# Kernel optimization log

Hardware: AMD Instinct MI355X
Metric: run time of the kernel (lower is better)

## Reference

```python
import jax, jax.numpy as jnp
import numpy as np

V, L, H, D, S, B = 32000, 6, 16, 1024, 512, 4
DK = D // H
DF = 4 * D
EPS = 1e-5


def setup_inputs() -> dict:
    key = jax.random.key(0)
    ks = jax.random.split(key, 24)
    std = 0.02
    def w(k, shape):
        return jax.random.normal(k, shape, dtype=jnp.float32) * std
    inp = {
        'x': jax.random.randint(ks[0], (B, S), 0, V),
        'tok_emb': w(ks[1], (V, D)),
        # per-layer params stacked on leading L axis; Linear stored as [in,out]
        'wq': w(ks[2], (L, D, D)), 'bq': jnp.zeros((L, D)),
        'wk': w(ks[3], (L, D, D)), 'bk': jnp.zeros((L, D)),
        'wv': w(ks[4], (L, D, D)), 'bv': jnp.zeros((L, D)),
        'wo': w(ks[5], (L, D, D)), 'bo': jnp.zeros((L, D)),
        'ln1_g': jnp.ones((L, D)), 'ln1_b': jnp.zeros((L, D)),
        'w1': w(ks[6], (L, D, DF)), 'b1': jnp.zeros((L, DF)),
        'w2': w(ks[7], (L, DF, D)), 'b2': jnp.zeros((L, D)),
        'ln2_g': jnp.ones((L, D)), 'ln2_b': jnp.zeros((L, D)),
        'lnf_g': jnp.ones((D,)), 'lnf_b': jnp.zeros((D,)),
        'lm_w': w(ks[8], (D, V)),
    }
    return inp


def _layernorm(x, g, b):
    mu = jnp.mean(x, axis=-1, keepdims=True)
    var = jnp.mean(jnp.square(x - mu), axis=-1, keepdims=True)
    return (x - mu) * jax.lax.rsqrt(var + EPS) * g + b


def _sinusoidal_pe(seq_len, d_model):
    pos = jnp.arange(seq_len, dtype=jnp.float32)[:, None]
    div = jnp.exp(jnp.arange(0, d_model, 2, dtype=jnp.float32) * (-np.log(10000.0) / d_model))
    pe = jnp.zeros((seq_len, d_model), dtype=jnp.float32)
    pe = pe.at[:, 0::2].set(jnp.sin(pos * div))
    pe = pe.at[:, 1::2].set(jnp.cos(pos * div))
    return pe  # [S, D]


def _gpt_forward(x, tok_emb, wq, bq, wk, bk, wv, bv, wo, bo,
                 ln1_g, ln1_b, w1, b1, w2, b2, ln2_g, ln2_b,
                 lnf_g, lnf_b, lm_w):
    b, s = x.shape
    h = tok_emb[x] + _sinusoidal_pe(s, D)  # [B,S,D]
    causal = jnp.tril(jnp.ones((s, s), dtype=bool))  # True = keep
    scale = 1.0 / np.sqrt(DK)

    def block(h, p):
        (wq, bq, wk, bk, wv, bv, wo, bo,
         ln1_g, ln1_b, w1, b1, w2, b2, ln2_g, ln2_b) = p
        hn = _layernorm(h, ln1_g, ln1_b)
        q = (hn @ wq + bq).reshape(b, s, H, DK)
        k = (hn @ wk + bk).reshape(b, s, H, DK)
        v = (hn @ wv + bv).reshape(b, s, H, DK)
        scores = jnp.einsum('bqhd,bkhd->bhqk', q, k) * scale
        scores = jnp.where(causal, scores, -1e9)
        attn = jax.nn.softmax(scores, axis=-1)
        ctx = jnp.einsum('bhqk,bkhd->bqhd', attn, v).reshape(b, s, D)
        h = h + (ctx @ wo + bo)
        hn2 = _layernorm(h, ln2_g, ln2_b)
        ff = jax.nn.gelu(hn2 @ w1 + b1, approximate=False) @ w2 + b2
        return h + ff, None

    params = (wq, bq, wk, bk, wv, bv, wo, bo,
              ln1_g, ln1_b, w1, b1, w2, b2, ln2_g, ln2_b)
    h, _ = jax.lax.scan(block, h, params)
    h = _layernorm(h, lnf_g, lnf_b)
    return h @ lm_w  # [B,S,V] logits


def reference(x, tok_emb, wq, bq, wk, bk, wv, bv, wo, bo,
              ln1_g, ln1_b, w1, b1, w2, b2, ln2_g, ln2_b,
              lnf_g, lnf_b, lm_w):
    return _gpt_forward(x, tok_emb, wq, bq, wk, bk, wv, bv, wo, bo,
                        ln1_g, ln1_b, w1, b1, w2, b2, ln2_g, ln2_b,
                        lnf_g, lnf_b, lm_w)
```

## Files before the change

### kernel.cpp

```cpp
#include <hip/hip_runtime.h>
#include <hip/hip_bf16.h>
#include <math.h>

#define V_SIZE 32000
#define L_NUM 6
#define H_NUM 16
#define D_MODEL 1024
#define S_LEN 512
#define B_SZ 4
#define DF_DIM 4096
#define ROWS (B_SZ * S_LEN)
#define QKV_N (3 * D_MODEL)
#define KVBLK 64
#define NJOB 12

typedef unsigned short u16;
typedef __attribute__((ext_vector_type(8))) short short8v;
typedef __attribute__((ext_vector_type(4))) float f32x4;

__device__ __forceinline__ float b2f(u16 b) {
  union { float f; unsigned u; } c; c.u = ((unsigned)b) << 16; return c.f;
}
__device__ __forceinline__ u16 f2b(float f) {
  __hip_bfloat16 h = __float2bfloat16(f);
  union { __hip_bfloat16 h; u16 u; } c; c.h = h; return c.u;
}
__device__ __forceinline__ void g2l16(const void* g, void* l) {
  __builtin_amdgcn_global_load_lds(
      (const __attribute__((address_space(1))) void*)g,
      (__attribute__((address_space(3))) void*)l, 16, 0, 0);
}

__global__ __launch_bounds__(256) void embed_kernel(
    const int* __restrict__ x, const float* __restrict__ tok_emb,
    float* __restrict__ h) {
  int row = blockIdx.x;
  int s = row % S_LEN;
  int tok = x[row];
  const float* te = tok_emb + (size_t)tok * D_MODEL;
  float* hr = h + (size_t)row * D_MODEL;
  float pos = (float)s;
  const float c = 9.210340371976184f / (float)D_MODEL;
#pragma unroll
  for (int i = 0; i < D_MODEL / 256; ++i) {
    int d = threadIdx.x + i * 256;
    float freq = expf(-(float)(d & ~1) * c);
    float ang = pos * freq;
    float pe = (d & 1) ? cosf(ang) : sinf(ang);
    hr[d] = te[d] + pe;
  }
}

__global__ __launch_bounds__(256) void layernorm_kernel(
    const float* __restrict__ in, const float* __restrict__ g,
    const float* __restrict__ b, u16* __restrict__ out) {
  const int row = blockIdx.x * 4 + (threadIdx.x >> 6);
  const int lane = threadIdx.x & 63;
  const float4* xr = (const float4*)(in + (size_t)row * D_MODEL);
  float4 v[4];
  float s1 = 0.f, s2 = 0.f;
#pragma unroll
  for (int i = 0; i < 4; ++i) {
    float4 t = xr[lane + i * 64];
    v[i] = t;
    s1 += t.x + t.y + t.z + t.w;
    s2 += t.x * t.x + t.y * t.y + t.z * t.z + t.w * t.w;
  }
#pragma unroll
  for (int off = 32; off; off >>= 1) {
    s1 += __shfl_xor(s1, off, 64);
    s2 += __shfl_xor(s2, off, 64);
  }
  const float mu = s1 * (1.0f / D_MODEL);
  const float var = s2 * (1.0f / D_MODEL) - mu * mu;
  const float rstd = rsqrtf(var + 1e-5f);
  u16* orow = out + (size_t)row * D_MODEL;
#pragma unroll
  for (int i = 0; i < 4; ++i) {
    const int d = (lane + i * 64) * 4;
    const float4 gv = *(const float4*)&g[d];
    const float4 bv = *(const float4*)&b[d];
    u16 o0 = f2b((v[i].x - mu) * rstd * gv.x + bv.x);
    u16 o1 = f2b((v[i].y - mu) * rstd * gv.y + bv.y);
    u16 o2 = f2b((v[i].z - mu) * rstd * gv.z + bv.z);
    u16 o3 = f2b((v[i].w - mu) * rstd * gv.w + bv.w);
    uint2 pk;
    pk.x = (unsigned)o0 | ((unsigned)o1 << 16);
    pk.y = (unsigned)o2 | ((unsigned)o3 << 16);
    *(uint2*)&orow[d] = pk;
  }
}

__global__ __launch_bounds__(256) void transpose_all(
    const float* __restrict__ wq, const float* __restrict__ wk,
    const float* __restrict__ wv, const float* __restrict__ wo,
    const float* __restrict__ w1, const float* __restrict__ w2,
    const float* __restrict__ lm_w,
    u16* __restrict__ wqkvT, u16* __restrict__ woT,
    u16* __restrict__ w1T, u16* __restrict__ w2T, u16* __restrict__ lmT) {
  const size_t DD = (size_t)D_MODEL * D_MODEL;
  const size_t DDF = (size_t)D_MODEL * DF_DIM;
  const long QS = (long)QKV_N * D_MODEL;
  int gid = blockIdx.x;
  const float* src;
  u16* dst;
  int K, N, kt, nt;
  if (gid < 12288) {
    const int l = gid / 2048, rjob = gid % 2048;
    const int which = rjob / 512, t = rjob % 512;
    kt = t % 16; nt = t / 16;
    K = D_MODEL; N = D_MODEL;
    src = (which == 0 ? wq : which == 1 ? wk : which == 2 ? wv : wo) + l * DD;
    dst = (which < 3) ? (wqkvT + l * QS + which * DD) : (woT + l * DD);
  } else if (gid < 24576) {
    const int idx = gid - 12288;
    const int l = idx / 2048, t = idx % 2048;
    kt = t % 16; nt = t / 16;
    K = D_MODEL; N = DF_DIM;
    src = w1 + l * DDF; dst = w1T + l * DDF;
  } else if (gid < 36864) {
    const int idx = gid - 24576;
    const int l = idx / 2048, t = idx % 2048;
    kt = t % 64; nt = t / 64;
    K = DF_DIM; N = D_MODEL;
    src = w2 + l * DDF; dst = w2T + l * DDF;
  } else {
    const int idx = gid - 36864;
    kt = idx % 16; nt = idx / 16;
    K = D_MODEL; N = V_SIZE;
    src = lm_w; dst = lmT;
  }
  __shared__ float t[64][33];
  const int n0 = nt * 32, k0 = kt * 64;
  const int tx = threadIdx.x & 31, ty = threadIdx.x >> 5;
#pragma unroll
  for (int i = 0; i < 64; i += 8)
    t[ty + i][tx] = src[(size_t)(k0 + ty + i) * N + n0 + tx];
  __syncthreads();
#pragma unroll
  for (int j = 0; j < 32; j += 8) {
    const int n = ty + j;
    u16 lo = f2b(t[2 * tx][n]);
    u16 hi = f2b(t[2 * tx + 1][n]);
    *(unsigned*)&dst[(size_t)(n0 + n) * K + k0 + 2 * tx] =
        (unsigned)lo | ((unsigned)hi << 16);
  }
}

__global__ __launch_bounds__(256) void pack_qkv_bias(
    const float* __restrict__ bq, const float* __restrict__ bk,
    const float* __restrict__ bv, float* __restrict__ out) {
  int i = blockIdx.x * 256 + threadIdx.x;
  int l = i / QKV_N, j = i % QKV_N;
  float v = (j < D_MODEL) ? bq[l * D_MODEL + j]
          : (j < 2 * D_MODEL) ? bk[l * D_MODEL + j - D_MODEL]
          : bv[l * D_MODEL + j - 2 * D_MODEL];
  out[i] = v;
}

template <int TM, int OUT_MODE, bool GELU_ACT, int SPLITK>
__global__ __launch_bounds__(256) void gemm_bf16(
    const u16* __restrict__ A, const u16* __restrict__ Bt,
    const float* __restrict__ bias, float* __restrict__ Cf,
    u16* __restrict__ Cb, int M, int N, int K) {
  constexpr int MF = TM / 32;
  constexpr int AINSTS = TM / 32;
  __shared__ __align__(16) u16 As[2][TM * 64];
  __shared__ __align__(16) u16 Bs[2][128 * 64];
  const int tid = threadIdx.x;
  const int wid = tid >> 6;
  const int lane = tid & 63;
  const int wr = wid >> 1, wc = wid & 1;
  const int nwg = gridDim.x;
  const int id = blockIdx.x;
  const int q = nwg >> 3, r = nwg & 7;
  const int xcd = id & 7, i0 = id >> 3;
  const int swz = (xcd < r ? xcd * (q + 1) : r * (q + 1) + (xcd - r) * q) + i0;
  const int kh = (SPLITK > 1) ? (swz & (SPLITK - 1)) : 0;
  const int rest = (SPLITK > 1) ? (swz >> 1) : swz;
  const int gm = M / TM;
  const int bm = rest % gm, bn = rest / gm;
  const int Ksub = K / SPLITK;
  const int rowi = lane >> 3;
  const int gsw = ((lane & 7) ^ rowi) * 8;
  const u16* Ag = A + (size_t)(bm * TM + wid * (TM / 4) + rowi) * K + kh * Ksub + gsw;
  const u16* Bg = Bt + (size_t)(bn * 128 + wid * 32 + rowi) * K + kh * Ksub + gsw;
  auto stage = [&](int buf, int k0) {
#pragma unroll
    for (int i = 0; i < AINSTS; ++i)
      g2l16(Ag + k0 + (size_t)(8 * i) * K, As[buf] + wid * (TM / 4) * 64 + i * 512);
#pragma unroll
    for (int i = 0; i < 4; ++i)
      g2l16(Bg + k0 + (size_t)(8 * i) * K, Bs[buf] + wid * 2048 + i * 512);
  };
  f32x4 acc[MF][4] = {};
  const int fr = lane & 15;
  const int hi = lane >> 4;
  stage(0, 0);
  __syncthreads();
  for (int k0 = 0; k0 < Ksub; k0 += 64) {
    const int cur = (k0 >> 6) & 1;
    if (k0 + 64 < Ksub) stage(cur ^ 1, k0 + 64);
    short8v a[MF][2], b[4][2];
#pragma unroll
    for (int m = 0; m < MF; ++m)
#pragma unroll
      for (int kk = 0; kk < 2; ++kk) {
        const int g = (kk * 4 + hi) ^ (fr & 7);
        a[m][kk] = *(const short8v*)&As[cur][(wr * (TM / 2) + m * 16 + fr) * 64 + g * 8];
      }
#pragma unroll
    for (int n = 0; n < 4; ++n)
#pragma unroll
      for (int kk = 0; kk < 2; ++kk) {
        const int g = (kk * 4 + hi) ^ (fr & 7);
        b[n][kk] = *(const short8v*)&Bs[cur][(wc * 64 + n * 16 + fr) * 64 + g * 8];
      }
    __builtin_amdgcn_s_setprio(1);
#pragma unroll
    for (int kk = 0; kk < 2; ++kk)
#pragma unroll
      for (int m = 0; m < MF; ++m)
#pragma unroll
        for (int n = 0; n < 4; ++n)
          acc[m][n] = __builtin_amdgcn_mfma_f32_16x16x32_bf16(a[m][kk], b[n][kk], acc[m][n], 0, 0, 0);
    __builtin_amdgcn_s_setprio(0);
    __syncthreads();
  }
  const int row0 = bm * TM + wr * (TM / 2) + hi * 4;
  const int col0 = bn * 128 + wc * 64 + fr;
#pragma unroll
  for (int m = 0; m < MF; ++m) {
#pragma unroll
    for (int n = 0; n < 4; ++n) {
      const int col = col0 + n * 16;
      float bv = (OUT_MODE == 2) ? 0.f : bias[col];
      if (SPLITK > 1 && kh != 0) bv = 0.f;
#pragma unroll
      for (int r2 = 0; r2 < 4; ++r2) {
        const int row = row0 + m * 16 + r2;
        float v = acc[m][n][r2] + bv;
        if (GELU_ACT) v = 0.5f * v * (1.0f + erff(v * 0.70710678118f));
        size_t idx = (size_t)row * N + col;
        if (OUT_MODE == 0) Cb[idx] = f2b(v);
        else if (OUT_MODE == 1) {
          if (SPLITK > 1) atomicAdd(&Cf[idx], v);
          else Cf[idx] += v;
        } else Cf[idx] = v;
      }
    }
  }
}

#define LDA_H(H)                                                            \
  _Pragma("unroll") for (int m = 0; m < 4; ++m)                             \
  _Pragma("unroll") for (int ks = 0; ks < 2; ++ks) {                        \
    const int row_ = wm * 128 + (H)*64 + m * 16 + fr;                       \
    const int g_ = (ks * 4 + hi) ^ (fr & 7);                                \
    a[m][ks] = *(const short8v*)&smem[cur * 16384 + row_ * 64 + g_ * 8];    \
  }
#define LDB_H(H)                                                            \
  _Pragma("unroll") for (int n = 0; n < 2; ++n)                             \
  _Pragma("unroll") for (int ks = 0; ks < 2; ++ks) {                        \
    const int row_ = wn * 64 + (H)*32 + n * 16 + fr;                        \
    const int g_ = (ks * 4 + hi) ^ (fr & 7);                                \
    b[n][ks] = *(const short8v*)&smem[32768 + cur * 16384 + row_ * 64 + g_ * 8]; \
  }
#define MFMA_CLUSTER(QA, QB)                                                \
  __builtin_amdgcn_s_barrier();                                             \
  asm volatile("s_waitcnt lgkmcnt(0)" ::: "memory");                        \
  __builtin_amdgcn_sched_barrier(0);                                        \
  __builtin_amdgcn_s_setprio(1);                                            \
  _Pragma("unroll") for (int ks = 0; ks < 2; ++ks)                          \
  _Pragma("unroll") for (int m = 0; m < 4; ++m)                             \
  _Pragma("unroll") for (int n = 0; n < 2; ++n)                             \
    acc[(QA)*4 + m][(QB)*2 + n] = __builtin_amdgcn_mfma_f32_16x16x32_bf16(  \
        a[m][ks], b[n][ks], acc[(QA)*4 + m][(QB)*2 + n], 0, 0, 0);          \
  __builtin_amdgcn_s_setprio(0);

__global__ __launch_bounds__(512, 2) void gemm256_lm(
    const u16* __restrict__ A, const u16* __restrict__ Bt,
    float* __restrict__ C, int M, int N, int K) {
  extern __shared__ __align__(16) u16 smem[];
  const int tid = threadIdx.x, wid = tid >> 6, lane = tid & 63;
  const int wm = wid >> 2, wn = wid & 3;
  const int fr = lane & 15, hi = lane >> 4;
  const int T = K / 64;
  const int nwg = gridDim.x, id = blockIdx.x;
  const int q = nwg >> 3, r = nwg & 7;
  const int xcd = id & 7, i0 = id >> 3;
  const int swz = (xcd < r ? xcd * (q + 1) : r * (q + 1) + (xcd - r) * q) + i0;
  const int gm = M / 256;
  const int bm = swz % gm, bn = swz / gm;
  const int rowA0 = bm * 256, rowB0 = bn * 256;
  const int rowoff = wid * 8 + (lane >> 3);
  const int gsw = ((lane & 7) ^ (lane >> 3)) * 8;
  auto stA = [&](int qq, int tt, int bb) {
    g2l16(A + (size_t)(rowA0 + qq * 64 + rowoff) * K + tt * 64 + gsw,
          smem + bb * 16384 + qq * 4096 + wid * 512);
  };
  auto stB = [&](int qq, int tt, int bb) {
    g2l16(Bt + (size_t)(rowB0 + qq * 64 + rowoff) * K + tt * 64 + gsw,
          smem + 32768 + bb * 16384 + qq * 4096 + wid * 512);
  };
  f32x4 acc[8][4] = {};
  stA(0, 0, 0); stA(2, 0, 0);
  stB(0, 0, 0); stB(1, 0, 0); stB(2, 0, 0); stB(3, 0, 0);
  stA(1, 0, 0); stA(3, 0, 0);
  if (T > 1) {
    stA(0, 1, 1); stA(2, 1, 1);
    asm volatile("s_waitcnt vmcnt(2)" ::: "memory");
  } else {
    asm volatile("s_waitcnt vmcnt(0)" ::: "memory");
  }
  __builtin_amdgcn_s_barrier();
  for (int t = 0; t < T; ++t) {
    const int cur = t & 1, nxt = cur ^ 1;
    short8v a[4][2], b[2][2];
    LDA_H(0); LDB_H(0);
    if (t + 1 < T) { stB(0, t + 1, nxt); stB(1, t + 1, nxt); }
    MFMA_CLUSTER(0, 0);
    __builtin_amdgcn_s_barrier();
    LDB_H(1);
    if (t + 1 < T) { stB(2, t + 1, nxt); stB(3, t + 1, nxt); }
    MFMA_CLUSTER(0, 1);
    __builtin_amdgcn_s_barrier();
    LDA_H(1);
    if (t + 1 < T) { stA(1, t + 1, nxt); stA(3, t + 1, nxt); }
    MFMA_CLUSTER(1, 1);
    __builtin_amdgcn_s_barrier();
    LDB_H(0);
    if (t + 2 < T) { stA(0, t + 2, cur); stA(2, t + 2, cur); }
    MFMA_CLUSTER(1, 0);
    if (t + 1 < T) {
      if (t + 2 < T) asm volatile("s_waitcnt vmcnt(2)" ::: "memory");
      else           asm volatile("s_waitcnt vmcnt(0)" ::: "memory");
      __builtin_amdgcn_s_barrier();
    }
  }
  float* lf = (float*)smem;
#pragma unroll
  for (int c = 0; c < 2; ++c) {
    __syncthreads();
    if (wm == c) {
#pragma unroll
      for (int m = 0; m < 8; ++m)
#pragma unroll
        for (int n = 0; n < 4; ++n)
#pragma unroll
          for (int rr = 0; rr < 4; ++rr)
            lf[(m * 16 + hi * 4 + rr) * 256 + wn * 64 + n * 16 + fr] =
                acc[m][n][rr];
    }
    __syncthreads();
#pragma unroll
    for (int i = 0; i < 16; ++i) {
      const int f = i * 2048 + tid * 4;
      const int rw = f >> 8, cl = f & 255;
      f32x4 v = *(const f32x4*)&lf[f];
      *(f32x4*)&C[(size_t)(rowA0 + c * 128 + rw) * N + rowB0 + cl] = v;
    }
  }
}

__global__ __launch_bounds__(256) void attn_part(
    const u16* __restrict__ qkv, float* __restrict__ Op,
    float* __restrict__ Ml, u16* __restrict__ ctx) {
  __shared__ __align__(16) u16 smem[3 * 64 * 72];
  u16 (*Qs)[72] = (u16(*)[72])smem;
  u16 (*Ks)[72] = (u16(*)[72])(smem + 4608);
  u16 (*Vs)[72] = (u16(*)[72])(smem + 9216);
  const int job = blockIdx.x, bh = blockIdx.y;
  constexpr int qt_of[NJOB] = {0, 1, 2, 3, 4, 4, 5, 5, 6, 6, 7, 7};
  constexpr int ch_of[NJOB] = {0, 0, 0, 0, 0, 1, 0, 1, 0, 1, 0, 1};
  const int qt = qt_of[job], ch = ch_of[job];
  const int b = bh >> 4, h = bh & 15;
  const int tid = threadIdx.x, wid = tid >> 6, lane = tid & 63;
  const int fr = lane & 15, ko = (lane >> 4) * 8;
  u16 (*Ps)[72] = (u16(*)[72])(smem + wid * 1152);
  const size_t rb = (size_t)b * S_LEN;
  const int q0 = qt * 64;
  const int hq = h * 64;
  const int t_lo = ch * 4;
  const int t_hi = (qt + 1 < t_lo + 4) ? qt + 1 : t_lo + 4;
#pragma unroll
  for (int i = 0; i < 2; ++i) {
    int e = tid + i * 256, r = e >> 3, c = (e & 7) * 8;
    *(short8v*)&Qs[r][c] = *(const short8v*)&qkv[(rb + q0 + r) * QKV_N + hq + c];
  }
  __syncthreads();
  short8v qf[2];
#pragma unroll
  for (int ks = 0; ks < 2; ++ks)
    qf[ks] = *(const short8v*)&Qs[wid * 16 + fr][ks * 32 + ko];
  f32x4 acc_o[4] = {};
  float mrow[4], lrow[4];
#pragma unroll
  for (int r = 0; r < 4; ++r) { mrow[r] = -1e30f; lrow[r] = 0.f; }
  short8v kreg[2], vreg[2];
  auto loadregs = [&](int t) {
    const int k0 = t * KVBLK;
#pragma unroll
    for (int i = 0; i < 2; ++i) {
      const int e = tid + i * 256, rr = e >> 3, cc = (e & 7) * 8;
      kreg[i] = *(const short8v*)&qkv[(rb + k0 + rr) * QKV_N + D_MODEL + hq + cc];
      vreg[i] = *(const short8v*)&qkv[(rb + k0 + rr) * QKV_N + 2 * D_MODEL + hq + cc];
    }
  };
  loadregs(t_lo);
  for (int t = t_lo; t < t_hi; ++t) {
    __syncthreads();
#pragma unroll
    for (int i = 0; i < 2; ++i) {
      const int e = tid + i * 256, rr = e >> 3, cc = (e & 7) * 8;
      *(short8v*)&Ks[rr][cc] = kreg[i];
#pragma unroll
      for (int j = 0; j < 8; ++j) Vs[cc + j][rr] = (u16)vreg[i][j];
    }
    __syncthreads();
    if (t + 1 < t_hi) loadregs(t + 1);
    const int k0 = t * KVBLK;
    f32x4 s[4] = {};
    __builtin_amdgcn_s_setprio(1);
#pragma unroll
    for (int n = 0; n < 4; ++n)
#pragma unroll
      for (int ks = 0; ks < 2; ++ks) {
        short8v kf = *(const short8v*)&Ks[n * 16 + fr][ks * 32 + ko];
        s[n] = __builtin_amdgcn_mfma_f32_16x16x32_bf16(qf[ks], kf, s[n], 0, 0, 0);
      }
    __builtin_amdgcn_s_setprio(0);
    const int rbase = q0 + wid * 16 + (lane >> 4) * 4;
#pragma unroll
    for (int r = 0; r < 4; ++r) {
      const int row_g = rbase + r;
      float vmax = -1e30f;
#pragma unroll
      for (int n = 0; n < 4; ++n) {
        float v = s[n][r] * 0.125f;
        if (k0 + n * 16 + fr > row_g) v = -1e30f;
        s[n][r] = v;
        vmax = fmaxf(vmax, v);
      }
#pragma unroll
      for (int off = 1; off < 16; off <<= 1) vmax = fmaxf(vmax, __shfl_xor(vmax, off, 64));
      const float mnew = fmaxf(mrow[r], vmax);
      const float sc = __expf(mrow[r] - mnew);
      mrow[r] = mnew;
      float ssum = 0.f;
#pragma unroll
      for (int n = 0; n < 4; ++n) {
        float p = __expf(s[n][r] - mnew);
        s[n][r] = p;
        ssum += p;
      }
#pragma unroll
      for (int off = 1; off < 16; off <<= 1) ssum += __shfl_xor(ssum, off, 64);
      lrow[r] = lrow[r] * sc + ssum;
#pragma unroll
      for (int n = 0; n < 4; ++n) {
        acc_o[n][r] *= sc;
        Ps[(lane >> 4) * 4 + r][n * 16 + fr] = f2b(s[n][r]);
      }
    }
    __builtin_amdgcn_s_setprio(1);
#pragma unroll
    for (int ks = 0; ks < 2; ++ks) {
      short8v pf = *(const short8v*)&Ps[fr][ks * 32 + ko];
#pragma unroll
      for (int n = 0; n < 4; ++n) {
        short8v vf = *(const short8v*)&Vs[n * 16 + fr][ks * 32 + ko];
        acc_o[n] = __builtin_amdgcn_mfma_f32_16x16x32_bf16(pf, vf, acc_o[n], 0, 0, 0);
      }
    }
    __builtin_amdgcn_s_setprio(0);
  }
  if (qt < 4) {
#pragma unroll
    for (int r = 0; r < 4; ++r) {
      const int row_l = wid * 16 + (lane >> 4) * 4 + r;
      const float inv = 1.0f / lrow[r];
#pragma unroll
      for (int n = 0; n < 4; ++n)
        ctx[(rb + q0 + row_l) * D_MODEL + hq + n * 16 + fr] = f2b(acc_o[n][r] * inv);
    }
  } else {
    const size_t jb = (size_t)(bh * NJOB + job);
#pragma unroll
    for (int r = 0; r < 4; ++r) {
      const int row_l = wid * 16 + (lane >> 4) * 4 + r;
      const size_t base = (jb * 64 + row_l) * 64;
#pragma unroll
      for (int n = 0; n < 4; ++n) Op[base + n * 16 + fr] = acc_o[n][r];
      if (fr == 0) {
        Ml[jb * 128 + row_l * 2] = mrow[r];
        Ml[jb * 128 + row_l * 2 + 1] = lrow[r];
      }
    }
  }
}

__global__ __launch_bounds__(256) void attn_combine(
    const float* __restrict__ Op, const float* __restrict__ Ml,
    u16* __restrict__ ctx) {
  const int qt = blockIdx.x + 4, bh = blockIdx.y;
  const int b = bh >> 4, h = bh & 15;
  const int j0 = 4 + blockIdx.x * 2;
  const size_t rb = (size_t)b * S_LEN;
  const int q0 = qt * 64, hq = h * 64;
  const size_t jb1 = (size_t)(bh * NJOB + j0);
  const size_t jb2 = jb1 + 1;
#pragma unroll
  for (int i = 0; i < 4; ++i) {
    const int idx4 = threadIdx.x + i * 256;
    const int row = idx4 >> 4, c4 = (idx4 & 15) * 4;
    f32x4 o1 = *(const f32x4*)&Op[(jb1 * 64 + row) * 64 + c4];
    const float m1 = Ml[jb1 * 128 + row * 2], l1 = Ml[jb1 * 128 + row * 2 + 1];
    f32x4 o2 = *(const f32x4*)&Op[(jb2 * 64 + row) * 64 + c4];
    const float m2 = Ml[jb2 * 128 + row * 2], l2 = Ml[jb2 * 128 + row * 2 + 1];
    const float m = fmaxf(m1, m2);
    const float e1 = __expf(m1 - m), e2 = __expf(m2 - m);
    const float inv = 1.0f / (l1 * e1 + l2 * e2);
    float o[4];
#pragma unroll
    for (int j = 0; j < 4; ++j) o[j] = o1[j] * e1 + o2[j] * e2;
    uint2 pk;
    pk.x = (unsigned)f2b(o[0] * inv) | ((unsigned)f2b(o[1] * inv) << 16);
    pk.y = (unsigned)f2b(o[2] * inv) | ((unsigned)f2b(o[3] * inv) << 16);
    *(uint2*)&ctx[(rb + q0 + row) * D_MODEL + hq + c4] = pk;
  }
}

extern "C" void kernel_launch(void* const* d_in, const int* in_sizes, int n_in,
                              void* d_out, int out_size, void* d_ws, size_t ws_size,
                              hipStream_t stream) {
  const int* x = (const int*)d_in[0];
  const float* tok_emb = (const float*)d_in[1];
  const float* wq = (const float*)d_in[2];
  const float* bq = (const float*)d_in[3];
  const float* wk = (const float*)d_in[4];
  const float* bk = (const float*)d_in[5];
  const float* wv = (const float*)d_in[6];
  const float* bv = (const float*)d_in[7];
  const float* wo = (const float*)d_in[8];
  const float* bo = (const float*)d_in[9];
  const float* ln1_g = (const float*)d_in[10];
  const float* ln1_b = (const float*)d_in[11];
  const float* w1 = (const float*)d_in[12];
  const float* b1 = (const float*)d_in[13];
  const float* w2 = (const float*)d_in[14];
  const float* b2 = (const float*)d_in[15];
  const float* ln2_g = (const float*)d_in[16];
  const float* ln2_b = (const float*)d_in[17];
  const float* lnf_g = (const float*)d_in[18];
  const float* lnf_b = (const float*)d_in[19];
  const float* lm_w = (const float*)d_in[20];

  char* w = (char*)d_ws;
  float* h    = (float*)(w);
  u16*  hn    = (u16*)(w + (8ll << 20));
  u16*  qkvb  = (u16*)(w + (12ll << 20));
  u16*  cbuf  = (u16*)(w + (24ll << 20));
  u16*  ff    = qkvb;
  u16*  wqkvT = (u16*)(w + (28ll << 20));
  u16*  woT   = (u16*)(w + (64ll << 20));
  u16*  w1T   = (u16*)(w + (76ll << 20));
  u16*  w2T   = (u16*)(w + (124ll << 20));
  u16*  lmT   = (u16*)(w + (172ll << 20));
  float* bqkv = (float*)(w + (235ll << 20));
  float* Op   = (float*)(w + (236ll << 20));
  float* Ml   = (float*)(w + (249ll << 20));

  transpose_all<<<52864, 256, 0, stream>>>(
      wq, wk, wv, wo, w1, w2, lm_w, wqkvT, woT, w1T, w2T, lmT);
  pack_qkv_bias<<<L_NUM * QKV_N / 256, 256, 0, stream>>>(bq, bk, bv, bqkv);

  embed_kernel<<<ROWS, 256, 0, stream>>>(x, tok_emb, h);

  const size_t DD = (size_t)D_MODEL * D_MODEL;
  const size_t DDF = (size_t)D_MODEL * DF_DIM;
  const long QS = (long)QKV_N * D_MODEL;
  const int nQKV = (ROWS / 64) * (QKV_N / 128);
  const int nPRJ = 2 * (ROWS / 64) * (D_MODEL / 128);
  const int nFF1 = (ROWS / 64) * (DF_DIM / 128);
  const int nFF2 = 2 * (ROWS / 64) * (D_MODEL / 128);
  for (int l = 0; l < L_NUM; ++l) {
    layernorm_kernel<<<ROWS / 4, 256, 0, stream>>>(h, ln1_g + l * D_MODEL, ln1_b + l * D_MODEL, hn);
    gemm_bf16<64, 0, false, 1><<<nQKV, 256, 0, stream>>>(
        hn, wqkvT + (size_t)l * QS, bqkv + l * QKV_N, nullptr, qkvb,
        ROWS, QKV_N, D_MODEL);
    attn_part<<<dim3(NJOB, B_SZ * H_NUM), 256, 0, stream>>>(qkvb, Op, Ml, cbuf);
    attn_combine<<<dim3(4, B_SZ * H_NUM), 256, 0, stream>>>(Op, Ml, cbuf);
    gemm_bf16<64, 1, false, 2><<<nPRJ, 256, 0, stream>>>(
        cbuf, woT + l * DD, bo + l * D_MODEL, h, nullptr, ROWS, D_MODEL, D_MODEL);
    layernorm_kernel<<<ROWS / 4, 256, 0, stream>>>(h, ln2_g + l * D_MODEL, ln2_b + l * D_MODEL, hn);
    gemm_bf16<64, 0, true, 1><<<nFF1, 256, 0, stream>>>(
        hn, w1T + l * DDF, b1 + l * DF_DIM, nullptr, ff, ROWS, DF_DIM, D_MODEL);
    gemm_bf16<64, 1, false, 2><<<nFF2, 256, 0, stream>>>(
        ff, w2T + l * DDF, b2 + l * D_MODEL, h, nullptr, ROWS, D_MODEL, DF_DIM);
  }
  layernorm_kernel<<<ROWS / 4, 256, 0, stream>>>(h, lnf_g, lnf_b, hn);

  hipFuncSetAttribute((const void*)gemm256_lm,
                      hipFuncAttributeMaxDynamicSharedMemorySize, 131072);
  const int nLM = (ROWS / 256) * (V_SIZE / 256);
  gemm256_lm<<<nLM, 512, 131072, stream>>>(
      hn, lmT, (float*)d_out, ROWS, V_SIZE, D_MODEL);
}
```

Measured before the change: 1.350 ms.

## Shrink LM-head GEMM tile to 128x256 with K=32 steps and higher occupancy

Replaces the 256x256 LM-head GEMM, which used 128KB of dynamic LDS and a K=64 pipelined schedule, with a 128x256 tile using K=32 steps and 48KB of static LDS. Launch bounds now allow 4 blocks per CU instead of 2, and the grid doubles. The goal is more resident waves and better latency hiding on the large vocab projection. In exchange, each block reuses less of its loaded data, a simpler double buffer waits on vmcnt(0) every iteration, and the fp32 output goes through LDS in four 32-row chunks.

```diff
diff --git a/kernel.cpp b/kernel.cpp
--- a/kernel.cpp
+++ b/kernel.cpp
@@ -252,113 +252,95 @@
   }
 }
 
-#define LDA_H(H)                                                            \
-  _Pragma("unroll") for (int m = 0; m < 4; ++m)                             \
-  _Pragma("unroll") for (int ks = 0; ks < 2; ++ks) {                        \
-    const int row_ = wm * 128 + (H)*64 + m * 16 + fr;                       \
-    const int g_ = (ks * 4 + hi) ^ (fr & 7);                                \
-    a[m][ks] = *(const short8v*)&smem[cur * 16384 + row_ * 64 + g_ * 8];    \
-  }
-#define LDB_H(H)                                                            \
-  _Pragma("unroll") for (int n = 0; n < 2; ++n)                             \
-  _Pragma("unroll") for (int ks = 0; ks < 2; ++ks) {                        \
-    const int row_ = wn * 64 + (H)*32 + n * 16 + fr;                        \
-    const int g_ = (ks * 4 + hi) ^ (fr & 7);                                \
-    b[n][ks] = *(const short8v*)&smem[32768 + cur * 16384 + row_ * 64 + g_ * 8]; \
-  }
-#define MFMA_CLUSTER(QA, QB)                                                \
-  __builtin_amdgcn_s_barrier();                                             \
-  asm volatile("s_waitcnt lgkmcnt(0)" ::: "memory");                        \
-  __builtin_amdgcn_sched_barrier(0);                                        \
-  __builtin_amdgcn_s_setprio(1);                                            \
-  _Pragma("unroll") for (int ks = 0; ks < 2; ++ks)                          \
-  _Pragma("unroll") for (int m = 0; m < 4; ++m)                             \
-  _Pragma("unroll") for (int n = 0; n < 2; ++n)                             \
-    acc[(QA)*4 + m][(QB)*2 + n] = __builtin_amdgcn_mfma_f32_16x16x32_bf16(  \
-        a[m][ks], b[n][ks], acc[(QA)*4 + m][(QB)*2 + n], 0, 0, 0);          \
-  __builtin_amdgcn_s_setprio(0);
-
-__global__ __launch_bounds__(512, 2) void gemm256_lm(
+__global__ __launch_bounds__(512, 4) void gemm_lm(
     const u16* __restrict__ A, const u16* __restrict__ Bt,
     float* __restrict__ C, int M, int N, int K) {
-  extern __shared__ __align__(16) u16 smem[];
+  __shared__ __align__(16) u16 smem[24576];
   const int tid = threadIdx.x, wid = tid >> 6, lane = tid & 63;
   const int wm = wid >> 2, wn = wid & 3;
   const int fr = lane & 15, hi = lane >> 4;
-  const int T = K / 64;
+  const int T = K / 32;
   const int nwg = gridDim.x, id = blockIdx.x;
   const int q = nwg >> 3, r = nwg & 7;
   const int xcd = id & 7, i0 = id >> 3;
   const int swz = (xcd < r ? xcd * (q + 1) : r * (q + 1) + (xcd - r) * q) + i0;
-  const int gm = M / 256;
+  const int gm = M / 128;
   const int bm = swz % gm, bn = swz / gm;
-  const int rowA0 = bm * 256, rowB0 = bn * 256;
-  const int rowoff = wid * 8 + (lane >> 3);
-  const int gsw = ((lane & 7) ^ (lane >> 3)) * 8;
-  auto stA = [&](int qq, int tt, int bb) {
-    g2l16(A + (size_t)(rowA0 + qq * 64 + rowoff) * K + tt * 64 + gsw,
-          smem + bb * 16384 + qq * 4096 + wid * 512);
+  const int rowA0 = bm * 128, rowB0 = bn * 256;
+  const int gsw = ((lane & 3) ^ ((lane >> 2) & 3)) * 8;
+  const u16* Ag = A + (size_t)(rowA0 + wid * 16 + (lane >> 2)) * K + gsw;
+  const u16* Bg = Bt + (size_t)(rowB0 + wid * 32 + (lane >> 2)) * K + gsw;
+  auto stage = [&](int buf, int t) {
+    g2l16(Ag + t * 32, smem + buf * 4096 + wid * 512);
+    g2l16(Bg + t * 32, smem + 8192 + buf * 8192 + wid * 1024);
+    g2l16(Bg + t * 32 + (size_t)16 * K, smem + 8192 + buf * 8192 + wid * 1024 + 512);
   };
-  auto stB = [&](int qq, int tt, int bb) {
-    g2l16(Bt + (size_t)(rowB0 + qq * 64 + rowoff) * K + tt * 64 + gsw,
-          smem + 32768 + bb * 16384 + qq * 4096 + wid * 512);
-  };
-  f32x4 acc[8][4] = {};
-  stA(0, 0, 0); stA(2, 0, 0);
-  stB(0, 0, 0); stB(1, 0, 0); stB(2, 0, 0); stB(3, 0, 0);
-  stA(1, 0, 0); stA(3, 0, 0);
-  if (T > 1) {
-    stA(0, 1, 1); stA(2, 1, 1);
-    asm volatile("s_waitcnt vmcnt(2)" ::: "memory");
-  } else {
-    asm volatile("s_waitcnt vmcnt(0)" ::: "memory");
-  }
+  f32x4 acc[4][4] = {};
+  stage(0, 0);
+  asm volatile("s_waitcnt vmcnt(0)" ::: "memory");
   __builtin_amdgcn_s_barrier();
   for (int t = 0; t < T; ++t) {
     const int cur = t & 1, nxt = cur ^ 1;
-    short8v a[4][2], b[2][2];
-    LDA_H(0); LDB_H(0);
-    if (t + 1 < T) { stB(0, t + 1, nxt); stB(1, t + 1, nxt); }
-    MFMA_CLUSTER(0, 0);
+    short8v a[4], b[4];
+    const int g = hi ^ (fr & 3);
+#pragma unroll
+    for (int m = 0; m < 4; ++m)
+      a[m] = *(const short8v*)&smem[cur * 4096 + (wm * 64 + m * 16 + fr) * 32 + g * 8];
+#pragma unroll
+    for (int n = 0; n < 2; ++n)
+      b[n] = *(const short8v*)&smem[8192 + cur * 8192 + (wn * 64 + n * 16 + fr) * 32 + g * 8];
+    if (t + 1 < T) stage(nxt, t + 1);
     __builtin_amdgcn_s_barrier();
-    LDB_H(1);
-    if (t + 1 < T) { stB(2, t + 1, nxt); stB(3, t + 1, nxt); }
-    MFMA_CLUSTER(0, 1);
+    asm volatile("s_waitcnt lgkmcnt(0)" ::: "memory");
+    __builtin_amdgcn_sched_barrier(0);
+    __builtin_amdgcn_s_setprio(1);
+#pragma unroll
+    for (int m = 0; m < 4; ++m)
+#pragma unroll
+      for (int n = 0; n < 2; ++n)
+        acc[m][n] = __builtin_amdgcn_mfma_f32_16x16x32_bf16(a[m], b[n], acc[m][n], 0, 0, 0);
+    __builtin_amdgcn_s_setprio(0);
     __builtin_amdgcn_s_barrier();
-    LDA_H(1);
-    if (t + 1 < T) { stA(1, t + 1, nxt); stA(3, t + 1, nxt); }
-    MFMA_CLUSTER(1, 1);
+#pragma unroll
+    for (int n = 2; n < 4; ++n)
+      b[n] = *(const short8v*)&smem[8192 + cur * 8192 + (wn * 64 + n * 16 + fr) * 32 + g * 8];
     __builtin_amdgcn_s_barrier();
-    LDB_H(0);
-    if (t + 2 < T) { stA(0, t + 2, cur); stA(2, t + 2, cur); }
-    MFMA_CLUSTER(1, 0);
+    asm volatile("s_waitcnt lgkmcnt(0)" ::: "memory");
+    __builtin_amdgcn_sched_barrier(0);
+    __builtin_amdgcn_s_setprio(1);
+#pragma unroll
+    for (int m = 0; m < 4; ++m)
+#pragma unroll
+      for (int n = 2; n < 4; ++n)
+        acc[m][n] = __builtin_amdgcn_mfma_f32_16x16x32_bf16(a[m], b[n], acc[m][n], 0, 0, 0);
+    __builtin_amdgcn_s_setprio(0);
     if (t + 1 < T) {
-      if (t + 2 < T) asm volatile("s_waitcnt vmcnt(2)" ::: "memory");
-      else           asm volatile("s_waitcnt vmcnt(0)" ::: "memory");
+      asm volatile("s_waitcnt vmcnt(0)" ::: "memory");
       __builtin_amdgcn_s_barrier();
     }
   }
   float* lf = (float*)smem;
 #pragma unroll
-  for (int c = 0; c < 2; ++c) {
+  for (int c = 0; c < 4; ++c) {
     __syncthreads();
-    if (wm == c) {
-#pragma unroll
-      for (int m = 0; m < 8; ++m)
+    if (wm == (c >> 1)) {
+      const int mbase = (c & 1) * 2;
+#pragma unroll
+      for (int mm = 0; mm < 2; ++mm)
 #pragma unroll
         for (int n = 0; n < 4; ++n)
 #pragma unroll
           for (int rr = 0; rr < 4; ++rr)
-            lf[(m * 16 + hi * 4 + rr) * 256 + wn * 64 + n * 16 + fr] =
-                acc[m][n][rr];
+            lf[(mm * 16 + hi * 4 + rr) * 256 + wn * 64 + n * 16 + fr] =
+                acc[mbase + mm][n][rr];
     }
     __syncthreads();
 #pragma unroll
-    for (int i = 0; i < 16; ++i) {
-      const int f = i * 2048 + tid * 4;
+    for (int i = 0; i < 4; ++i) {
+      const int f = (i * 512 + tid) * 4;
       const int rw = f >> 8, cl = f & 255;
       f32x4 v = *(const f32x4*)&lf[f];
-      *(f32x4*)&C[(size_t)(rowA0 + c * 128 + rw) * N + rowB0 + cl] = v;
+      *(f32x4*)&C[(size_t)(rowA0 + c * 32 + rw) * N + rowB0 + cl] = v;
     }
   }
 }
@@ -601,9 +583,7 @@
   }
   layernorm_kernel<<<ROWS / 4, 256, 0, stream>>>(h, lnf_g, lnf_b, hn);
 
-  hipFuncSetAttribute((const void*)gemm256_lm,
-                      hipFuncAttributeMaxDynamicSharedMemorySize, 131072);
-  const int nLM = (ROWS / 256) * (V_SIZE / 256);
-  gemm256_lm<<<nLM, 512, 131072, stream>>>(
+  const int nLM = (ROWS / 128) * (V_SIZE / 256);
+  gemm_lm<<<nLM, 512, 0, stream>>>(
       hn, lmT, (float*)d_out, ROWS, V_SIZE, D_MODEL);
 }
```

Result: no change. 1.366 ms (+1.2%).
